# Kernel tuning notes

Measured on AMD Instinct MI355X. Metric: run time of the kernel, lower is better.

## Reference

```python
import jax, jax.numpy as jnp
import numpy as np
from jax.scipy.ndimage import map_coordinates

ANGLES = 180
PROJ = 180
IMG = 256
THETA_RAD = np.deg2rad(np.linspace(0.0, 180.0, ANGLES, endpoint=False)).astype(np.float32)


def _ramp_filter(size):
    # skimage _get_fourier_filter(size, 'ramp')
    n = np.concatenate((np.arange(1, size // 2 + 1, 2),
                        np.arange(size // 2 - 1, 0, -2)))
    f = np.zeros(size)
    f[0] = 0.25
    f[1::2] = -1.0 / (np.pi * n) ** 2
    return (2.0 * np.real(np.fft.fft(f))).astype(np.float32)


def radon_t(img, theta):
    # skimage radon(circle=True): rotate by each angle (bilinear warp) and sum rows
    N = img.shape[0]
    center = N // 2
    y, x = jnp.mgrid[0:N, 0:N]
    x = x.astype(jnp.float32)
    y = y.astype(jnp.float32)

    def one(th):
        c, s = jnp.cos(th), jnp.sin(th)
        sx = c * x + s * y - center * (c + s - 1.0)   # source col
        sy = -s * x + c * y - center * (c - s - 1.0)  # source row
        rot = map_coordinates(img, [sy, sx], order=1, mode='constant', cval=0.0)
        return rot.sum(axis=0)  # sum over rows -> [N]

    cols = jax.vmap(one)(theta)  # [A, N]
    return cols.T                # [N, A] sinogram


def iradon_t(sino, theta):
    # skimage iradon(circle=True, filter='ramp', interpolation='linear')
    N, A = sino.shape
    pad = max(64, int(2 ** np.ceil(np.log2(2 * N))))
    filt = jnp.asarray(_ramp_filter(pad))
    proj = jnp.fft.fft(jnp.pad(sino, ((0, pad - N), (0, 0))), axis=0) * filt[:, None]
    filtered = jnp.real(jnp.fft.ifft(proj, axis=0)[:N, :]).astype(jnp.float32)  # [N, A]

    radius = N // 2
    xpr, ypr = jnp.mgrid[0:N, 0:N]
    xpr = (xpr - radius).astype(jnp.float32)
    ypr = (ypr - radius).astype(jnp.float32)

    def one(col, th):
        # detector coordinate t, shifted so index 0 corresponds to x[0] = -N//2
        t = ypr * jnp.cos(th) - xpr * jnp.sin(th) + radius
        i0 = jnp.floor(t).astype(jnp.int32)
        frac = t - i0
        v0 = col[jnp.clip(i0, 0, N - 1)]
        v1 = col[jnp.clip(i0 + 1, 0, N - 1)]
        val = (1.0 - frac) * v0 + frac * v1
        inb = (t >= 0.0) & (t <= N - 1.0)  # np.interp(..., left=0, right=0)
        return jnp.where(inb, val, 0.0)

    back = jax.vmap(one)(filtered.T, theta).sum(axis=0)  # [N, N]
    mask = (xpr ** 2 + ypr ** 2) <= radius ** 2
    return jnp.where(mask, back, 0.0) * (jnp.pi / (2.0 * A))


def setup_inputs() -> dict:
    key = jax.random.key(0)
    ks = jax.random.split(key, 7)
    scale = 1.0 / np.sqrt(PROJ)
    return {
        "x": jax.random.normal(ks[0], (4, 3, IMG, IMG), dtype=jnp.float32),
        "Wq": jax.random.normal(ks[1], (PROJ, PROJ), dtype=jnp.float32) * scale,
        "bq": jax.random.normal(ks[2], (PROJ,), dtype=jnp.float32) * scale,
        "Wk": jax.random.normal(ks[3], (PROJ, PROJ), dtype=jnp.float32) * scale,
        "bk": jax.random.normal(ks[4], (PROJ,), dtype=jnp.float32) * scale,
        "Wv": jax.random.normal(ks[5], (PROJ, PROJ), dtype=jnp.float32) * scale,
        "bv": jax.random.normal(ks[6], (PROJ,), dtype=jnp.float32) * scale,
    }


def reference(x, Wq, bq, Wk, bk, Wv, bv):
    B, C, H, W = x.shape
    theta = jnp.asarray(THETA_RAD)
    imgs = x.reshape(B * C, H, W)
    sino = jax.vmap(lambda im: radon_t(im, theta))(imgs)  # [BC, H, A]
    Q = sino @ Wq.T + bq
    K = sino @ Wk.T + bk
    V = sino @ Wv.T + bv
    scores = jax.nn.softmax(
        jnp.einsum('nij,nkj->nik', Q, K) / jnp.sqrt(jnp.float32(PROJ)), axis=-1)
    att = jnp.einsum('nik,nkj->nij', scores, V)            # [BC, H, A]
    rec = jax.vmap(lambda s: iradon_t(s, theta))(att)      # [BC, H, W]
    return rec.reshape(B, C, H, W)
```

## Files before the change

kernel.cpp:

```cpp
#include <hip/hip_runtime.h>

#define AANG 180
#define NN 256
#define BCH 12

#ifndef M_PI
#define M_PI 3.14159265358979323846
#endif

__device__ __forceinline__ int iclamp(int v, int lo, int hi) {
    return v < lo ? lo : (v > hi ? hi : v);
}

#define LSTR 259
#define LROWSMAX 130

__global__ __launch_bounds__(1024, 1)
void radon_kernel(const float* __restrict__ x, float* __restrict__ partial) {
    __shared__ float tile[LROWSMAX * LSTR];
    __shared__ float red[2][1024];
    int blk = blockIdx.x;
    int g = blk % 30;
    int t = blk / 30;
    int h = t & 1;
    int n = t >> 1;
    int tid = threadIdx.x;
    int lx = tid & 255;
    int qid = tid >> 8;
    int R0 = h ? 127 : -1;
    int nrows = h ? 130 : 129;
    unsigned lrmax = h ? 128u : 127u;
    const float* img = x + (size_t)n * NN * NN;

    for (int rr = qid; rr < nrows; rr += 4) {
        int gr = R0 + rr;
        bool rok = (gr >= 0) && (gr < NN);
        const float* row = img + gr * NN;
        int gc = lx - 1;
        tile[rr * LSTR + lx] = (rok && gc >= 0) ? row[gc] : 0.0f;
        if (lx < 3) {
            int gc2 = 255 + lx;
            tile[rr * LSTR + 256 + lx] = (rok && gc2 < NN) ? row[gc2] : 0.0f;
        }
    }
    __syncthreads();

    float fx = (float)lx;
    int ubase = qid * 64;

    for (int pp = 0; pp < 3; ++pp) {
        int a0 = g + (2 * pp) * 30;
        int a1 = a0 + 30;
        float th0 = (float)((double)a0 * (M_PI / 180.0));
        float th1 = (float)((double)a1 * (M_PI / 180.0));
        float c0 = cosf(th0), s0 = sinf(th0);
        float c1 = cosf(th1), s1 = sinf(th1);
        float kx0 = -128.0f * (c0 + s0 - 1.0f), ky0 = -128.0f * (c0 - s0 - 1.0f);
        float kx1 = -128.0f * (c1 + s1 - 1.0f), ky1 = -128.0f * (c1 - s1 - 1.0f);
        float xcon0 = c0 * fx + kx0;
        float dcon0 = -s0 * fx + ky0;
        float xcon1 = c1 * fx + kx1;
        float dcon1 = -s1 * fx + ky1;
        float acc0 = 0.0f, acc1 = 0.0f;
#pragma unroll 4
        for (int i = 0; i < 64; ++i) {
            float fy = (float)(ubase + i);
            float sy0 = __builtin_fmaf(c0, fy, dcon0);
            float sx0 = __builtin_fmaf(s0, fy, xcon0);
            float sy1 = __builtin_fmaf(c1, fy, dcon1);
            float sx1 = __builtin_fmaf(s1, fy, xcon1);
            float iyf0 = floorf(sy0), ixf0 = floorf(sx0);
            float iyf1 = floorf(sy1), ixf1 = floorf(sx1);
            int lr0 = (int)iyf0 - R0, lc0 = (int)ixf0 + 1;
            int lr1 = (int)iyf1 - R0, lc1 = (int)ixf1 + 1;
            if ((unsigned)lr0 <= lrmax && (unsigned)lc0 <= 256u) {
                float wy = sy0 - iyf0, wx = sx0 - ixf0;
                const float* t0 = &tile[lr0 * LSTR + lc0];
                float v00 = t0[0], v01 = t0[1];
                float v10 = t0[LSTR], v11 = t0[LSTR + 1];
                float wx1 = 1.0f - wx, wy1 = 1.0f - wy;
                acc0 += wy1 * (wx1 * v00 + wx * v01) + wy * (wx1 * v10 + wx * v11);
            }
            if ((unsigned)lr1 <= lrmax && (unsigned)lc1 <= 256u) {
                float wy = sy1 - iyf1, wx = sx1 - ixf1;
                const float* t1 = &tile[lr1 * LSTR + lc1];
                float v00 = t1[0], v01 = t1[1];
                float v10 = t1[LSTR], v11 = t1[LSTR + 1];
                float wx1 = 1.0f - wx, wy1 = 1.0f - wy;
                acc1 += wy1 * (wx1 * v00 + wx * v01) + wy * (wx1 * v10 + wx * v11);
            }
        }
        if (pp) __syncthreads();
        red[0][tid] = acc0;
        red[1][tid] = acc1;
        __syncthreads();
        if (tid < 256) {
            float r0 = red[0][tid] + red[0][tid + 256] + red[0][tid + 512] + red[0][tid + 768];
            float r1 = red[1][tid] + red[1][tid + 256] + red[1][tid + 512] + red[1][tid + 768];
            size_t base = (((size_t)h * BCH + n) * AANG);
            partial[(base + a0) * NN + tid] = r0;
            partial[(base + a1) * NN + tid] = r1;
        }
    }
}

__global__ void wtrans_kernel(const float* __restrict__ Wq, const float* __restrict__ Wk,
                              const float* __restrict__ Wv, float* __restrict__ WqT,
                              float* __restrict__ WkT, float* __restrict__ WvT) {
    int idx = blockIdx.x * 256 + threadIdx.x;
    if (idx < AANG * AANG) {
        int p = idx / AANG;
        int j = idx - p * AANG;
        int src = j * AANG + p;
        WqT[idx] = Wq[src];
        WkT[idx] = Wk[src];
        WvT[idx] = Wv[src];
    }
}

__global__ void qkv_kernel(const float* __restrict__ partial,
                           const float* __restrict__ WqT, const float* __restrict__ bq,
                           const float* __restrict__ WkT, const float* __restrict__ bk,
                           const float* __restrict__ WvT, const float* __restrict__ bv,
                           float* __restrict__ Q, float* __restrict__ Kt,
                           float* __restrict__ V) {
    __shared__ float srow_t[AANG][8];
    int blk = blockIdx.x;
    int n = blk >> 5;
    int i0 = (blk & 31) * 8;
    int tid = threadIdx.x;
    const size_t HOFF = (size_t)BCH * AANG * NN;
    if (tid < AANG) {
        size_t idx = (((size_t)n) * AANG + tid) * NN + i0;
        float4 p0 = *(const float4*)&partial[idx];
        float4 p1 = *(const float4*)&partial[idx + 4];
        float4 q0 = *(const float4*)&partial[idx + HOFF];
        float4 q1 = *(const float4*)&partial[idx + HOFF + 4];
        srow_t[tid][0] = p0.x + q0.x;
        srow_t[tid][1] = p0.y + q0.y;
        srow_t[tid][2] = p0.z + q0.z;
        srow_t[tid][3] = p0.w + q0.w;
        srow_t[tid][4] = p1.x + q1.x;
        srow_t[tid][5] = p1.y + q1.y;
        srow_t[tid][6] = p1.z + q1.z;
        srow_t[tid][7] = p1.w + q1.w;
    }
    __syncthreads();
    if (tid < AANG) {
        int j = tid;
        float aq[8], ak[8], av[8];
        float bqv = bq[j], bkv = bk[j], bvv = bv[j];
        for (int r = 0; r < 8; ++r) { aq[r] = bqv; ak[r] = bkv; av[r] = bvv; }
#pragma unroll 2
        for (int p = 0; p < AANG; ++p) {
            float wq = WqT[p * AANG + j];
            float wk = WkT[p * AANG + j];
            float wv = WvT[p * AANG + j];
            float4 sv0 = *(const float4*)&srow_t[p][0];
            float4 sv1 = *(const float4*)&srow_t[p][4];
            aq[0] += sv0.x * wq; ak[0] += sv0.x * wk; av[0] += sv0.x * wv;
            aq[1] += sv0.y * wq; ak[1] += sv0.y * wk; av[1] += sv0.y * wv;
            aq[2] += sv0.z * wq; ak[2] += sv0.z * wk; av[2] += sv0.z * wv;
            aq[3] += sv0.w * wq; ak[3] += sv0.w * wk; av[3] += sv0.w * wv;
            aq[4] += sv1.x * wq; ak[4] += sv1.x * wk; av[4] += sv1.x * wv;
            aq[5] += sv1.y * wq; ak[5] += sv1.y * wk; av[5] += sv1.y * wv;
            aq[6] += sv1.z * wq; ak[6] += sv1.z * wk; av[6] += sv1.z * wv;
            aq[7] += sv1.w * wq; ak[7] += sv1.w * wk; av[7] += sv1.w * wv;
        }
        for (int r = 0; r < 8; ++r) {
            size_t qb = ((size_t)(n * NN + i0 + r)) * AANG + j;
            Q[qb] = aq[r];
            V[qb] = av[r];
        }
        size_t kb = ((size_t)(n * AANG + j)) * NN + i0;
        for (int r = 0; r < 8; ++r) Kt[kb + r] = ak[r];
    }
}

__global__ void attn_kernel(const float* __restrict__ Q, const float* __restrict__ Kt,
                            const float* __restrict__ V, float* __restrict__ att_t) {
    __shared__ float qrow[4][AANG];
    __shared__ float prob[4][NN];
    __shared__ float wm[4][4], wsm[4][4];
    int blk = blockIdx.x;
    int n = blk >> 6;
    int i0 = (blk & 63) * 4;
    int tid = threadIdx.x;
    int wid = tid >> 6;
    if (tid < AANG) {
#pragma unroll
        for (int r = 0; r < 4; ++r)
            qrow[r][tid] = Q[((size_t)(n * NN + i0 + r)) * AANG + tid];
    }
    __syncthreads();
    float d0 = 0.0f, d1 = 0.0f, d2 = 0.0f, d3 = 0.0f;
    const float* kb = Kt + (size_t)n * AANG * NN + tid;
#pragma unroll 4
    for (int j = 0; j < AANG; ++j) {
        float kv = kb[(size_t)j * NN];
        d0 += qrow[0][j] * kv;
        d1 += qrow[1][j] * kv;
        d2 += qrow[2][j] * kv;
        d3 += qrow[3][j] * kv;
    }
    const float rs = 0.0745355992f;
    float l0 = d0 * rs, l1 = d1 * rs, l2 = d2 * rs, l3 = d3 * rs;
    float m0 = l0, m1 = l1, m2 = l2, m3 = l3;
    for (int off = 32; off > 0; off >>= 1) {
        m0 = fmaxf(m0, __shfl_xor(m0, off));
        m1 = fmaxf(m1, __shfl_xor(m1, off));
        m2 = fmaxf(m2, __shfl_xor(m2, off));
        m3 = fmaxf(m3, __shfl_xor(m3, off));
    }
    if ((tid & 63) == 0) { wm[0][wid] = m0; wm[1][wid] = m1; wm[2][wid] = m2; wm[3][wid] = m3; }
    __syncthreads();
    float mx0 = fmaxf(fmaxf(wm[0][0], wm[0][1]), fmaxf(wm[0][2], wm[0][3]));
    float mx1 = fmaxf(fmaxf(wm[1][0], wm[1][1]), fmaxf(wm[1][2], wm[1][3]));
    float mx2 = fmaxf(fmaxf(wm[2][0], wm[2][1]), fmaxf(wm[2][2], wm[2][3]));
    float mx3 = fmaxf(fmaxf(wm[3][0], wm[3][1]), fmaxf(wm[3][2], wm[3][3]));
    float e0 = expf(l0 - mx0), e1 = expf(l1 - mx1);
    float e2 = expf(l2 - mx2), e3 = expf(l3 - mx3);
    float s0 = e0, s1 = e1, s2 = e2, s3 = e3;
    for (int off = 32; off > 0; off >>= 1) {
        s0 += __shfl_xor(s0, off);
        s1 += __shfl_xor(s1, off);
        s2 += __shfl_xor(s2, off);
        s3 += __shfl_xor(s3, off);
    }
    if ((tid & 63) == 0) { wsm[0][wid] = s0; wsm[1][wid] = s1; wsm[2][wid] = s2; wsm[3][wid] = s3; }
    __syncthreads();
    float dn0 = wsm[0][0] + wsm[0][1] + wsm[0][2] + wsm[0][3];
    float dn1 = wsm[1][0] + wsm[1][1] + wsm[1][2] + wsm[1][3];
    float dn2 = wsm[2][0] + wsm[2][1] + wsm[2][2] + wsm[2][3];
    float dn3 = wsm[3][0] + wsm[3][1] + wsm[3][2] + wsm[3][3];
    prob[0][tid] = e0 / dn0;
    prob[1][tid] = e1 / dn1;
    prob[2][tid] = e2 / dn2;
    prob[3][tid] = e3 / dn3;
    __syncthreads();
    if (tid < AANG) {
        float a0 = 0.0f, a1 = 0.0f, a2 = 0.0f, a3 = 0.0f;
        const float* vb = V + (size_t)n * NN * AANG + tid;
#pragma unroll 4
        for (int k = 0; k < NN; ++k) {
            float v = vb[(size_t)k * AANG];
            a0 += prob[0][k] * v;
            a1 += prob[1][k] * v;
            a2 += prob[2][k] * v;
            a3 += prob[3][k] * v;
        }
        float4 st = make_float4(a0, a1, a2, a3);
        *(float4*)&att_t[((size_t)(n * AANG + tid)) * NN + i0] = st;
    }
}

__global__ void filter_kernel(const float* __restrict__ att_t, float* __restrict__ filt) {
    __shared__ float col[NN];
    __shared__ float coef[128];
    int blk = blockIdx.x;
    int tid = threadIdx.x;
    col[tid] = att_t[(size_t)blk * NN + tid];
    if (tid < 128) {
        float d = (float)(2 * tid + 1);
        coef[tid] = -2.0f / ((float)(M_PI * M_PI) * d * d);
    }
    __syncthreads();
    float acc = 0.5f * col[tid];
#pragma unroll 4
    for (int m = 0; m < 128; ++m) {
        int d = 2 * m + 1;
        float lo = (tid - d >= 0) ? col[tid - d] : 0.0f;
        float hi = (tid + d < NN) ? col[tid + d] : 0.0f;
        acc += coef[m] * (lo + hi);
    }
    filt[(size_t)blk * NN + tid] = acc;
}

#define ACH 36
__global__ __launch_bounds__(1024)
void backproj_kernel(const float* __restrict__ filt, float* __restrict__ out) {
    __shared__ float cols[ACH][NN];
    __shared__ float cs[AANG], sn[AANG];
    int blk = blockIdx.x;
    int n = blk >> 6;
    int rg = blk & 63;
    int tid = threadIdx.x;
    int col = tid & 255;
    int rslot = tid >> 8;
    int r = rg * 4 + rslot;
    if (tid < AANG) {
        float th = (float)((double)tid * (M_PI / 180.0));
        cs[tid] = cosf(th);
        sn[tid] = sinf(th);
    }
    float xr = (float)(r - 128);
    float yr = (float)(col - 128);
    float acc = 0.0f;
    const float* fb = filt + (size_t)n * AANG * NN;
    for (int ch = 0; ch < AANG / ACH; ++ch) {
        __syncthreads();
        for (int idx = tid; idx < ACH * NN; idx += 1024) {
            int q = idx >> 8;
            int cc = idx & 255;
            cols[q][cc] = fb[(size_t)(ch * ACH + q) * NN + cc];
        }
        __syncthreads();
#pragma unroll 4
        for (int q = 0; q < ACH; ++q) {
            int aa = ch * ACH + q;
            float t = yr * cs[aa] - xr * sn[aa] + 128.0f;
            float i0f = floorf(t);
            int i0 = (int)i0f;
            float frac = t - i0f;
            int c0 = iclamp(i0, 0, NN - 1);
            int c1 = iclamp(i0 + 1, 0, NN - 1);
            float val = (1.0f - frac) * cols[q][c0] + frac * cols[q][c1];
            if (t >= 0.0f && t <= 255.0f) acc += val;
        }
    }
    bool inside = (xr * xr + yr * yr) <= 16384.0f;
    out[((size_t)(n * NN + r)) * NN + col] = inside ? acc * (float)(M_PI / 360.0) : 0.0f;
}

extern "C" void kernel_launch(void* const* d_in, const int* in_sizes, int n_in,
                              void* d_out, int out_size, void* d_ws, size_t ws_size,
                              hipStream_t stream) {
    const float* x  = (const float*)d_in[0];
    const float* Wq = (const float*)d_in[1];
    const float* bq = (const float*)d_in[2];
    const float* Wk = (const float*)d_in[3];
    const float* bk = (const float*)d_in[4];
    const float* Wv = (const float*)d_in[5];
    const float* bv = (const float*)d_in[6];
    float* out = (float*)d_out;
    float* ws = (float*)d_ws;

    const size_t SZ = (size_t)BCH * NN * AANG;
    float* P     = ws;
    float* Q     = P + 2 * SZ;
    float* Kt    = Q + SZ;
    float* V     = Kt + SZ;
    float* att_t = V + SZ;
    float* WqT   = att_t;
    float* WkT   = WqT + AANG * AANG;
    float* WvT   = WkT + AANG * AANG;
    float* filt  = P;

    wtrans_kernel<<<(AANG * AANG + 255) / 256, 256, 0, stream>>>(Wq, Wk, Wv, WqT, WkT, WvT);
    radon_kernel<<<BCH * 2 * 30, 1024, 0, stream>>>(x, P);
    qkv_kernel<<<BCH * (NN / 8), 256, 0, stream>>>(P, WqT, bq, WkT, bk, WvT, bv, Q, Kt, V);
    attn_kernel<<<BCH * (NN / 4), NN, 0, stream>>>(Q, Kt, V, att_t);
    filter_kernel<<<BCH * AANG, NN, 0, stream>>>(att_t, filt);
    backproj_kernel<<<BCH * (NN / 4), 1024, 0, stream>>>(filt, out);
}
```

Before: 463.4 us.

## Skip out-of-tile row segments in radon; remove clamps via padded shared buffers

In the radon kernel, each wave now works out the range of row indices whose rotated sample coordinates can fall inside its shared-memory tile, for both angles. It skips 16-row segments outside that range, which avoids many iterations that only fail the bounds test. The filter kernel zero-pads its shared column so the inner convolution loop no longer needs per-tap bounds checks. The backprojection kernel stores each column edge-padded to 384 entries so the interpolation indexing needs no clamps. The padding uses more shared memory, and the skip bounds rely on approximate float margins.

```diff
diff --git a/kernel.cpp b/kernel.cpp
--- a/kernel.cpp
+++ b/kernel.cpp
@@ -30,6 +30,8 @@
     int R0 = h ? 127 : -1;
     int nrows = h ? 130 : 129;
     unsigned lrmax = h ? 128u : 127u;
+    float Ylo = h ? 127.0f : -1.0f;
+    float Yhi1 = h ? 256.0f : 127.0f;
     const float* img = x + (size_t)n * NN * NN;
 
     for (int rr = qid; rr < nrows; rr += 4) {
@@ -47,6 +49,9 @@
 
     float fx = (float)lx;
     int ubase = qid * 64;
+    int wave = tid >> 6;
+    float fxA = (float)((wave & 3) * 64);
+    float fxB = fxA + 63.0f;
 
     for (int pp = 0; pp < 3; ++pp) {
         int a0 = g + (2 * pp) * 30;
@@ -61,33 +66,85 @@
         float dcon0 = -s0 * fx + ky0;
         float xcon1 = c1 * fx + kx1;
         float dcon1 = -s1 * fx + ky1;
+
+        float lo0, hi0, lo1, hi1;
+        {
+            float loY, hiY;
+            if (__builtin_fabsf(c0) > 1e-5f) {
+                float dA = -s0 * fxA + ky0, dB = -s0 * fxB + ky0;
+                float t1 = (Ylo - dA) / c0, t2 = (Yhi1 - dA) / c0;
+                float t3 = (Ylo - dB) / c0, t4 = (Yhi1 - dB) / c0;
+                loY = fminf(fminf(t1, t2), fminf(t3, t4));
+                hiY = fmaxf(fmaxf(t1, t2), fmaxf(t3, t4));
+            } else { loY = 0.0f; hiY = 256.0f; }
+            float loX, hiX;
+            if (s0 > 1e-5f) {
+                float xA = c0 * fxA + kx0, xB = c0 * fxB + kx0;
+                float t1 = (-1.0f - xA) / s0, t2 = (257.0f - xA) / s0;
+                float t3 = (-1.0f - xB) / s0, t4 = (257.0f - xB) / s0;
+                loX = fminf(fminf(t1, t2), fminf(t3, t4));
+                hiX = fmaxf(fmaxf(t1, t2), fmaxf(t3, t4));
+            } else { loX = 0.0f; hiX = 256.0f; }
+            lo0 = fmaxf(fmaxf(loY, loX) - 2.0f, 0.0f);
+            hi0 = fminf(fminf(hiY, hiX) + 3.0f, 256.0f);
+        }
+        {
+            float loY, hiY;
+            if (__builtin_fabsf(c1) > 1e-5f) {
+                float dA = -s1 * fxA + ky1, dB = -s1 * fxB + ky1;
+                float t1 = (Ylo - dA) / c1, t2 = (Yhi1 - dA) / c1;
+                float t3 = (Ylo - dB) / c1, t4 = (Yhi1 - dB) / c1;
+                loY = fminf(fminf(t1, t2), fminf(t3, t4));
+                hiY = fmaxf(fmaxf(t1, t2), fmaxf(t3, t4));
+            } else { loY = 0.0f; hiY = 256.0f; }
+            float loX, hiX;
+            if (s1 > 1e-5f) {
+                float xA = c1 * fxA + kx1, xB = c1 * fxB + kx1;
+                float t1 = (-1.0f - xA) / s1, t2 = (257.0f - xA) / s1;
+                float t3 = (-1.0f - xB) / s1, t4 = (257.0f - xB) / s1;
+                loX = fminf(fminf(t1, t2), fminf(t3, t4));
+                hiX = fmaxf(fmaxf(t1, t2), fmaxf(t3, t4));
+            } else { loX = 0.0f; hiX = 256.0f; }
+            lo1 = fmaxf(fmaxf(loY, loX) - 2.0f, 0.0f);
+            hi1 = fminf(fminf(hiY, hiX) + 3.0f, 256.0f);
+        }
+        int umin = (int)fminf(lo0, lo1);
+        int umax = (int)fmaxf(hi0, hi1);
+        umin = __builtin_amdgcn_readfirstlane(umin);
+        umax = __builtin_amdgcn_readfirstlane(umax);
+
         float acc0 = 0.0f, acc1 = 0.0f;
+#pragma unroll
+        for (int st = 0; st < 4; ++st) {
+            int t0i = ubase + st * 16;
+            if (t0i + 16 <= umin || t0i >= umax) continue;
 #pragma unroll 4
-        for (int i = 0; i < 64; ++i) {
-            float fy = (float)(ubase + i);
-            float sy0 = __builtin_fmaf(c0, fy, dcon0);
-            float sx0 = __builtin_fmaf(s0, fy, xcon0);
-            float sy1 = __builtin_fmaf(c1, fy, dcon1);
-            float sx1 = __builtin_fmaf(s1, fy, xcon1);
-            float iyf0 = floorf(sy0), ixf0 = floorf(sx0);
-            float iyf1 = floorf(sy1), ixf1 = floorf(sx1);
-            int lr0 = (int)iyf0 - R0, lc0 = (int)ixf0 + 1;
-            int lr1 = (int)iyf1 - R0, lc1 = (int)ixf1 + 1;
-            if ((unsigned)lr0 <= lrmax && (unsigned)lc0 <= 256u) {
-                float wy = sy0 - iyf0, wx = sx0 - ixf0;
-                const float* t0 = &tile[lr0 * LSTR + lc0];
-                float v00 = t0[0], v01 = t0[1];
-                float v10 = t0[LSTR], v11 = t0[LSTR + 1];
-                float wx1 = 1.0f - wx, wy1 = 1.0f - wy;
-                acc0 += wy1 * (wx1 * v00 + wx * v01) + wy * (wx1 * v10 + wx * v11);
-            }
-            if ((unsigned)lr1 <= lrmax && (unsigned)lc1 <= 256u) {
-                float wy = sy1 - iyf1, wx = sx1 - ixf1;
-                const float* t1 = &tile[lr1 * LSTR + lc1];
-                float v00 = t1[0], v01 = t1[1];
-                float v10 = t1[LSTR], v11 = t1[LSTR + 1];
-                float wx1 = 1.0f - wx, wy1 = 1.0f - wy;
-                acc1 += wy1 * (wx1 * v00 + wx * v01) + wy * (wx1 * v10 + wx * v11);
+            for (int i = 0; i < 16; ++i) {
+                float fy = (float)(t0i + i);
+                float sy0 = __builtin_fmaf(c0, fy, dcon0);
+                float sx0 = __builtin_fmaf(s0, fy, xcon0);
+                float sy1 = __builtin_fmaf(c1, fy, dcon1);
+                float sx1 = __builtin_fmaf(s1, fy, xcon1);
+                float iyf0 = floorf(sy0), ixf0 = floorf(sx0);
+                float iyf1 = floorf(sy1), ixf1 = floorf(sx1);
+                int lr0 = (int)iyf0 - R0, lc0 = (int)ixf0 + 1;
+                int lr1 = (int)iyf1 - R0, lc1 = (int)ixf1 + 1;
+                if ((unsigned)lr0 <= lrmax && (unsigned)lc0 <= 256u) {
+                    float wy = sy0 - iyf0, wx = sx0 - ixf0;
+                    const float* t0p = &tile[lr0 * LSTR + lc0];
+                    float v00 = t0p[0], v01 = t0p[1];
+                    float v10 = t0p[LSTR], v11 = t0p[LSTR + 1];
+                    float wx1 = 1.0f - wx, wy1 = 1.0f - wy;
+                    acc0 += wy1 * (wx1 * v00 + wx * v01) + wy * (wx1 * v10 + wx * v11);
+                }
+                if ((unsigned)lr1 <= lrmax && (unsigned)lc1 <= 256u) {
+                    float wy = sy1 - iyf1, wx = sx1 - ixf1;
+                    const float* t1p = &tile[lr1 * LSTR + lc1];
+                    float v00 = t1p[0], v01 = t1p[1];
+                    float v10 = t1p[LSTR], v11 = t1p[LSTR + 1];
+                    float wx1 = 1.0f - wx, wy1 = 1.0f - wy;
+                    acc1 += wy1 * (wx1 * v00 + wx * v01) + wy * (wx1 * v10 + wx * v11);
+                }
             }
         }
         if (pp) __syncthreads();
@@ -255,31 +312,33 @@
 }
 
 __global__ void filter_kernel(const float* __restrict__ att_t, float* __restrict__ filt) {
-    __shared__ float col[NN];
+    __shared__ float scol[512];
     __shared__ float coef[128];
     int blk = blockIdx.x;
     int tid = threadIdx.x;
-    col[tid] = att_t[(size_t)blk * NN + tid];
+    const float* src = &att_t[(size_t)blk * NN];
+    scol[tid] = (tid >= 128) ? src[tid - 128] : 0.0f;
+    scol[tid + 256] = (tid < 128) ? src[tid + 128] : 0.0f;
     if (tid < 128) {
         float d = (float)(2 * tid + 1);
         coef[tid] = -2.0f / ((float)(M_PI * M_PI) * d * d);
     }
     __syncthreads();
-    float acc = 0.5f * col[tid];
+    const float* c = &scol[tid + 128];
+    float acc = 0.5f * c[0];
 #pragma unroll 4
     for (int m = 0; m < 128; ++m) {
         int d = 2 * m + 1;
-        float lo = (tid - d >= 0) ? col[tid - d] : 0.0f;
-        float hi = (tid + d < NN) ? col[tid + d] : 0.0f;
-        acc += coef[m] * (lo + hi);
+        acc += coef[m] * (c[-d] + c[d]);
     }
     filt[(size_t)blk * NN + tid] = acc;
 }
 
 #define ACH 36
+#define BPW 384
 __global__ __launch_bounds__(1024)
 void backproj_kernel(const float* __restrict__ filt, float* __restrict__ out) {
-    __shared__ float cols[ACH][NN];
+    __shared__ float cols[ACH][BPW];
     __shared__ float cs[AANG], sn[AANG];
     int blk = blockIdx.x;
     int n = blk >> 6;
@@ -299,10 +358,11 @@
     const float* fb = filt + (size_t)n * AANG * NN;
     for (int ch = 0; ch < AANG / ACH; ++ch) {
         __syncthreads();
-        for (int idx = tid; idx < ACH * NN; idx += 1024) {
-            int q = idx >> 8;
-            int cc = idx & 255;
-            cols[q][cc] = fb[(size_t)(ch * ACH + q) * NN + cc];
+        for (int idx = tid; idx < ACH * BPW; idx += 1024) {
+            int q = idx / BPW;
+            int cc = idx - q * BPW;
+            int srci = iclamp(cc - 64, 0, NN - 1);
+            cols[q][cc] = fb[(size_t)(ch * ACH + q) * NN + srci];
         }
         __syncthreads();
 #pragma unroll 4
@@ -312,9 +372,9 @@
             float i0f = floorf(t);
             int i0 = (int)i0f;
             float frac = t - i0f;
-            int c0 = iclamp(i0, 0, NN - 1);
-            int c1 = iclamp(i0 + 1, 0, NN - 1);
-            float val = (1.0f - frac) * cols[q][c0] + frac * cols[q][c1];
+            const float* p = &cols[q][i0 + 64];
+            float v0 = p[0], v1 = p[1];
+            float val = (1.0f - frac) * v0 + frac * v1;
             if (t >= 0.0f && t <= 255.0f) acc += val;
         }
     }
```

New measurement: 483.7 us. 4.4% more time.

## Store K row-major and V transposed, process 8 query rows per attention block

Applied to the files above, without the earlier changes.

The QKV kernel now writes K in row-major [n,i,j] and V transposed so the attention kernel can read each thread's K row and V row as contiguous float4 loads. Each attention block handles 8 query rows instead of 4, halving the grid and reusing each K/V load across more rows. The filter kernel pads the column in shared memory to drop the bounds checks in its inner loop. The contiguous per-thread row reads stride by a full row across lanes, which may hurt coalescing compared with the earlier column-style access.

```diff
diff --git a/kernel.cpp b/kernel.cpp
--- a/kernel.cpp
+++ b/kernel.cpp
@@ -122,8 +122,8 @@
                            const float* __restrict__ WqT, const float* __restrict__ bq,
                            const float* __restrict__ WkT, const float* __restrict__ bk,
                            const float* __restrict__ WvT, const float* __restrict__ bv,
-                           float* __restrict__ Q, float* __restrict__ Kt,
-                           float* __restrict__ V) {
+                           float* __restrict__ Q, float* __restrict__ K,
+                           float* __restrict__ Vt) {
     __shared__ float srow_t[AANG][8];
     int blk = blockIdx.x;
     int n = blk >> 5;
@@ -151,7 +151,7 @@
         float aq[8], ak[8], av[8];
         float bqv = bq[j], bkv = bk[j], bvv = bv[j];
         for (int r = 0; r < 8; ++r) { aq[r] = bqv; ak[r] = bkv; av[r] = bvv; }
-#pragma unroll 2
+#pragma unroll 4
         for (int p = 0; p < AANG; ++p) {
             float wq = WqT[p * AANG + j];
             float wk = WkT[p * AANG + j];
@@ -170,108 +170,124 @@
         for (int r = 0; r < 8; ++r) {
             size_t qb = ((size_t)(n * NN + i0 + r)) * AANG + j;
             Q[qb] = aq[r];
-            V[qb] = av[r];
-        }
-        size_t kb = ((size_t)(n * AANG + j)) * NN + i0;
-        for (int r = 0; r < 8; ++r) Kt[kb + r] = ak[r];
-    }
-}
-
-__global__ void attn_kernel(const float* __restrict__ Q, const float* __restrict__ Kt,
-                            const float* __restrict__ V, float* __restrict__ att_t) {
-    __shared__ float qrow[4][AANG];
-    __shared__ float prob[4][NN];
-    __shared__ float wm[4][4], wsm[4][4];
-    int blk = blockIdx.x;
-    int n = blk >> 6;
-    int i0 = (blk & 63) * 4;
+            K[qb] = ak[r];
+        }
+        size_t vb = ((size_t)(n * AANG + j)) * NN + i0;
+        float4 v0 = make_float4(av[0], av[1], av[2], av[3]);
+        float4 v1 = make_float4(av[4], av[5], av[6], av[7]);
+        *(float4*)&Vt[vb] = v0;
+        *(float4*)&Vt[vb + 4] = v1;
+    }
+}
+
+__global__ void attn_kernel(const float* __restrict__ Q, const float* __restrict__ K,
+                            const float* __restrict__ Vt, float* __restrict__ att_t) {
+    __shared__ float qrow[8][AANG];
+    __shared__ float prob[8][NN];
+    __shared__ float wm[8][4], wsm[8][4];
+    int blk = blockIdx.x;
+    int n = blk >> 5;
+    int i0 = (blk & 31) * 8;
     int tid = threadIdx.x;
     int wid = tid >> 6;
     if (tid < AANG) {
 #pragma unroll
-        for (int r = 0; r < 4; ++r)
+        for (int r = 0; r < 8; ++r)
             qrow[r][tid] = Q[((size_t)(n * NN + i0 + r)) * AANG + tid];
     }
     __syncthreads();
-    float d0 = 0.0f, d1 = 0.0f, d2 = 0.0f, d3 = 0.0f;
-    const float* kb = Kt + (size_t)n * AANG * NN + tid;
-#pragma unroll 4
-    for (int j = 0; j < AANG; ++j) {
-        float kv = kb[(size_t)j * NN];
-        d0 += qrow[0][j] * kv;
-        d1 += qrow[1][j] * kv;
-        d2 += qrow[2][j] * kv;
-        d3 += qrow[3][j] * kv;
+    float d[8];
+#pragma unroll
+    for (int r = 0; r < 8; ++r) d[r] = 0.0f;
+    const float* krow = K + ((size_t)(n * NN) + tid) * AANG;
+#pragma unroll 3
+    for (int jj = 0; jj < AANG / 4; ++jj) {
+        float4 kv = *(const float4*)&krow[jj * 4];
+#pragma unroll
+        for (int r = 0; r < 8; ++r) {
+            float4 qv = *(const float4*)&qrow[r][jj * 4];
+            d[r] += qv.x * kv.x;
+            d[r] += qv.y * kv.y;
+            d[r] += qv.z * kv.z;
+            d[r] += qv.w * kv.w;
+        }
     }
     const float rs = 0.0745355992f;
-    float l0 = d0 * rs, l1 = d1 * rs, l2 = d2 * rs, l3 = d3 * rs;
-    float m0 = l0, m1 = l1, m2 = l2, m3 = l3;
+    float l[8], m[8], e[8], s[8];
+#pragma unroll
+    for (int r = 0; r < 8; ++r) { l[r] = d[r] * rs; m[r] = l[r]; }
     for (int off = 32; off > 0; off >>= 1) {
-        m0 = fmaxf(m0, __shfl_xor(m0, off));
-        m1 = fmaxf(m1, __shfl_xor(m1, off));
-        m2 = fmaxf(m2, __shfl_xor(m2, off));
-        m3 = fmaxf(m3, __shfl_xor(m3, off));
-    }
-    if ((tid & 63) == 0) { wm[0][wid] = m0; wm[1][wid] = m1; wm[2][wid] = m2; wm[3][wid] = m3; }
-    __syncthreads();
-    float mx0 = fmaxf(fmaxf(wm[0][0], wm[0][1]), fmaxf(wm[0][2], wm[0][3]));
-    float mx1 = fmaxf(fmaxf(wm[1][0], wm[1][1]), fmaxf(wm[1][2], wm[1][3]));
-    float mx2 = fmaxf(fmaxf(wm[2][0], wm[2][1]), fmaxf(wm[2][2], wm[2][3]));
-    float mx3 = fmaxf(fmaxf(wm[3][0], wm[3][1]), fmaxf(wm[3][2], wm[3][3]));
-    float e0 = expf(l0 - mx0), e1 = expf(l1 - mx1);
-    float e2 = expf(l2 - mx2), e3 = expf(l3 - mx3);
-    float s0 = e0, s1 = e1, s2 = e2, s3 = e3;
+#pragma unroll
+        for (int r = 0; r < 8; ++r) m[r] = fmaxf(m[r], __shfl_xor(m[r], off));
+    }
+    if ((tid & 63) == 0) {
+#pragma unroll
+        for (int r = 0; r < 8; ++r) wm[r][wid] = m[r];
+    }
+    __syncthreads();
+#pragma unroll
+    for (int r = 0; r < 8; ++r) {
+        float mx = fmaxf(fmaxf(wm[r][0], wm[r][1]), fmaxf(wm[r][2], wm[r][3]));
+        e[r] = expf(l[r] - mx);
+        s[r] = e[r];
+    }
     for (int off = 32; off > 0; off >>= 1) {
-        s0 += __shfl_xor(s0, off);
-        s1 += __shfl_xor(s1, off);
-        s2 += __shfl_xor(s2, off);
-        s3 += __shfl_xor(s3, off);
-    }
-    if ((tid & 63) == 0) { wsm[0][wid] = s0; wsm[1][wid] = s1; wsm[2][wid] = s2; wsm[3][wid] = s3; }
-    __syncthreads();
-    float dn0 = wsm[0][0] + wsm[0][1] + wsm[0][2] + wsm[0][3];
-    float dn1 = wsm[1][0] + wsm[1][1] + wsm[1][2] + wsm[1][3];
-    float dn2 = wsm[2][0] + wsm[2][1] + wsm[2][2] + wsm[2][3];
-    float dn3 = wsm[3][0] + wsm[3][1] + wsm[3][2] + wsm[3][3];
-    prob[0][tid] = e0 / dn0;
-    prob[1][tid] = e1 / dn1;
-    prob[2][tid] = e2 / dn2;
-    prob[3][tid] = e3 / dn3;
-    __syncthreads();
-    if (tid < AANG) {
-        float a0 = 0.0f, a1 = 0.0f, a2 = 0.0f, a3 = 0.0f;
-        const float* vb = V + (size_t)n * NN * AANG + tid;
-#pragma unroll 4
-        for (int k = 0; k < NN; ++k) {
-            float v = vb[(size_t)k * AANG];
-            a0 += prob[0][k] * v;
-            a1 += prob[1][k] * v;
-            a2 += prob[2][k] * v;
-            a3 += prob[3][k] * v;
-        }
-        float4 st = make_float4(a0, a1, a2, a3);
-        *(float4*)&att_t[((size_t)(n * AANG + tid)) * NN + i0] = st;
+#pragma unroll
+        for (int r = 0; r < 8; ++r) s[r] += __shfl_xor(s[r], off);
+    }
+    if ((tid & 63) == 0) {
+#pragma unroll
+        for (int r = 0; r < 8; ++r) wsm[r][wid] = s[r];
+    }
+    __syncthreads();
+#pragma unroll
+    for (int r = 0; r < 8; ++r) {
+        float dn = wsm[r][0] + wsm[r][1] + wsm[r][2] + wsm[r][3];
+        prob[r][tid] = e[r] / dn;
+    }
+    __syncthreads();
+    if (tid < AANG) {
+        float a[8];
+#pragma unroll
+        for (int r = 0; r < 8; ++r) a[r] = 0.0f;
+        const float* vrow = Vt + ((size_t)(n * AANG) + tid) * NN;
+#pragma unroll 4
+        for (int kk = 0; kk < NN / 4; ++kk) {
+            float4 v4 = *(const float4*)&vrow[kk * 4];
+#pragma unroll
+            for (int r = 0; r < 8; ++r) {
+                float4 p4 = *(const float4*)&prob[r][kk * 4];
+                a[r] += p4.x * v4.x;
+                a[r] += p4.y * v4.y;
+                a[r] += p4.z * v4.z;
+                a[r] += p4.w * v4.w;
+            }
+        }
+        size_t ob = ((size_t)(n * AANG + tid)) * NN + i0;
+        *(float4*)&att_t[ob] = make_float4(a[0], a[1], a[2], a[3]);
+        *(float4*)&att_t[ob + 4] = make_float4(a[4], a[5], a[6], a[7]);
     }
 }
 
 __global__ void filter_kernel(const float* __restrict__ att_t, float* __restrict__ filt) {
-    __shared__ float col[NN];
+    __shared__ float scol[512];
     __shared__ float coef[128];
     int blk = blockIdx.x;
     int tid = threadIdx.x;
-    col[tid] = att_t[(size_t)blk * NN + tid];
+    const float* src = &att_t[(size_t)blk * NN];
+    scol[tid] = (tid >= 128) ? src[tid - 128] : 0.0f;
+    scol[tid + 256] = (tid < 128) ? src[tid + 128] : 0.0f;
     if (tid < 128) {
         float d = (float)(2 * tid + 1);
         coef[tid] = -2.0f / ((float)(M_PI * M_PI) * d * d);
     }
     __syncthreads();
-    float acc = 0.5f * col[tid];
+    const float* c = &scol[tid + 128];
+    float acc = 0.5f * c[0];
 #pragma unroll 4
     for (int m = 0; m < 128; ++m) {
         int d = 2 * m + 1;
-        float lo = (tid - d >= 0) ? col[tid - d] : 0.0f;
-        float hi = (tid + d < NN) ? col[tid + d] : 0.0f;
-        acc += coef[m] * (lo + hi);
+        acc += coef[m] * (c[-d] + c[d]);
     }
     filt[(size_t)blk * NN + tid] = acc;
 }
@@ -338,9 +354,9 @@
     const size_t SZ = (size_t)BCH * NN * AANG;
     float* P     = ws;
     float* Q     = P + 2 * SZ;
-    float* Kt    = Q + SZ;
-    float* V     = Kt + SZ;
-    float* att_t = V + SZ;
+    float* K     = Q + SZ;
+    float* Vt    = K + SZ;
+    float* att_t = Vt + SZ;
     float* WqT   = att_t;
     float* WkT   = WqT + AANG * AANG;
     float* WvT   = WkT + AANG * AANG;
@@ -348,8 +364,8 @@
 
     wtrans_kernel<<<(AANG * AANG + 255) / 256, 256, 0, stream>>>(Wq, Wk, Wv, WqT, WkT, WvT);
     radon_kernel<<<BCH * 2 * 30, 1024, 0, stream>>>(x, P);
-    qkv_kernel<<<BCH * (NN / 8), 256, 0, stream>>>(P, WqT, bq, WkT, bk, WvT, bv, Q, Kt, V);
-    attn_kernel<<<BCH * (NN / 4), NN, 0, stream>>>(Q, Kt, V, att_t);
+    qkv_kernel<<<BCH * (NN / 8), 256, 0, stream>>>(P, WqT, bq, WkT, bk, WvT, bv, Q, K, Vt);
+    attn_kernel<<<BCH * (NN / 8), 256, 0, stream>>>(Q, K, Vt, att_t);
     filter_kernel<<<BCH * AANG, NN, 0, stream>>>(att_t, filt);
     backproj_kernel<<<BCH * (NN / 4), 1024, 0, stream>>>(filt, out);
 }
```

Measured after the change: 448.6 us. 1.03x faster.
